# Performance work log

Hardware: AMD Instinct MI355X
Metric: run time of the kernel (lower is better)

## Reference

```python
import jax, jax.numpy as jnp
import numpy as np

N_NODES = 100000
N_EDGES = 800000
N_GRAPHS = 4000
EMB = 128      # node_emb_dims
HID = 256      # hidden_dims
FP = 2048      # fingerprint_dims
FIELD_DIMS = {"atom_type": 120, "degree": 12, "charge": 10}


def setup_inputs() -> dict:
    key = jax.random.key(0)
    ks = iter(jax.random.split(key, 40))
    p = lambda shape: jax.random.normal(next(ks), shape, dtype=jnp.float32) * 0.02
    inp = {
        "atom_idx": jax.random.randint(next(ks), (N_NODES,), 0, FIELD_DIMS["atom_type"]),
        "degree_idx": jax.random.randint(next(ks), (N_NODES,), 0, FIELD_DIMS["degree"]),
        "charge_idx": jax.random.randint(next(ks), (N_NODES,), 0, FIELD_DIMS["charge"]),
        "edge_index": jax.random.randint(next(ks), (2, N_EDGES), 0, N_NODES),
        "batch": jnp.sort(jax.random.randint(next(ks), (N_NODES,), 0, N_GRAPHS)),
        "fingerprint": jax.random.normal(next(ks), (N_GRAPHS, FP), dtype=jnp.float32),
        # FFM projector params
        "emb_atom": p((FIELD_DIMS["atom_type"], EMB)),
        "emb_degree": p((FIELD_DIMS["degree"], EMB)),
        "emb_charge": p((FIELD_DIMS["charge"], EMB)),
        "proj_w1": p((3 * EMB, EMB)), "proj_b1": jnp.zeros((EMB,), jnp.float32),
        "proj_w2": p((EMB, EMB)), "proj_b2": jnp.zeros((EMB,), jnp.float32),
        # fingerprint linear
        "fp_w": p((FP, HID)), "fp_b": jnp.zeros((HID,), jnp.float32),
        # GCN layers
        "conv_w0": p((EMB, HID)), "conv_b0": jnp.zeros((HID,), jnp.float32),
        "conv_w1": p((HID, HID)), "conv_b1": jnp.zeros((HID,), jnp.float32),
        "conv_w2": p((HID, HID)), "conv_b2": jnp.zeros((HID,), jnp.float32),
        "conv_w3": p((HID, HID)), "conv_b3": jnp.zeros((HID,), jnp.float32),
        # head
        "lin1_w": p((2 * HID, HID // 2)), "lin1_b": jnp.zeros((HID // 2,), jnp.float32),
        "lin2_w": p((HID // 2, 1)), "lin2_b": jnp.zeros((1,), jnp.float32),
    }
    return inp


def gcn_conv(x, w, b, src, dst, n):
    # PyG GCNConv: linear, add self-loops, symmetric norm, scatter-add at dst, + bias
    xw = x @ w
    loop = jnp.arange(n)
    src_f = jnp.concatenate([src, loop])
    dst_f = jnp.concatenate([dst, loop])
    deg = jax.ops.segment_sum(jnp.ones_like(dst_f, dtype=x.dtype), dst_f, num_segments=n)
    dinv = jax.lax.rsqrt(deg)  # deg >= 1 thanks to self-loops
    norm = dinv[src_f] * dinv[dst_f]                       # [E+N]
    msg = xw[src_f] * norm[:, None]                        # [E+N, HID]
    return jax.ops.segment_sum(msg, dst_f, num_segments=n) + b


def reference(atom_idx, degree_idx, charge_idx, edge_index, batch, fingerprint,
              emb_atom, emb_degree, emb_charge,
              proj_w1, proj_b1, proj_w2, proj_b2, fp_w, fp_b,
              conv_w0, conv_b0, conv_w1, conv_b1, conv_w2, conv_b2, conv_w3, conv_b3,
              lin1_w, lin1_b, lin2_w, lin2_b):
    # FieldAwareFactorizationMachine projector (vectorized over all nodes)
    e = jnp.concatenate([emb_atom[atom_idx], emb_degree[degree_idx], emb_charge[charge_idx]], axis=-1)
    h = jax.nn.relu(e @ proj_w1 + proj_b1) @ proj_w2 + proj_b2   # [N, EMB]
    src, dst = edge_index[0], edge_index[1]
    for w, b in ((conv_w0, conv_b0), (conv_w1, conv_b1), (conv_w2, conv_b2), (conv_w3, conv_b3)):
        h = jax.nn.relu(gcn_conv(h, w, b, src, dst, N_NODES))
    pooled = jax.ops.segment_sum(h, batch, num_segments=N_GRAPHS)  # scatter sum pooling
    fp_emb = fingerprint @ fp_w + fp_b
    z = jnp.concatenate([fp_emb, pooled], axis=-1)                 # [B, 2*HID]
    z = jax.nn.relu(z @ lin1_w + lin1_b)
    return z @ lin2_w + lin2_b                                     # [B, 1]
```

## Files before the change

kernel.cpp:

```cpp
#include <hip/hip_runtime.h>
#include <stdint.h>

#define NN 100000
#define NE 800000
#define NG 4000
#define NBLK ((NN + 255) / 256)

typedef __attribute__((ext_vector_type(8))) short s16x8;
typedef __attribute__((ext_vector_type(4))) float f32x4;
typedef __attribute__((ext_vector_type(2))) float f32x2;

__device__ __forceinline__ float b2f(unsigned short u) {
    return __uint_as_float(((unsigned int)u) << 16);
}
__device__ __forceinline__ unsigned short f2b(float f) {
    unsigned int x = __float_as_uint(f);
    x = x + 0x7FFFu + ((x >> 16) & 1u);
    return (unsigned short)(x >> 16);
}
__device__ __forceinline__ s16x8 cvt8(const float* __restrict__ p) {
    float4 a = *(const float4*)p;
    float4 b = *(const float4*)(p + 4);
    s16x8 r = {(short)f2b(a.x), (short)f2b(a.y), (short)f2b(a.z), (short)f2b(a.w),
               (short)f2b(b.x), (short)f2b(b.y), (short)f2b(b.z), (short)f2b(b.w)};
    return r;
}

__device__ __forceinline__ void gload16(const void* g, void* l) {
    __builtin_amdgcn_global_load_lds((const __attribute__((address_space(1))) unsigned int*)g,
                                     (__attribute__((address_space(3))) unsigned int*)l, 16, 0, 0);
}

__device__ __forceinline__ void acc8(f32x2* acc, s16x8 r) {
    const unsigned int* u = (const unsigned int*)&r;
#pragma unroll
    for (int q = 0; q < 4; ++q) {
        unsigned int w = u[q];
        f32x2 x;
        x[0] = __uint_as_float(w << 16);
        x[1] = __uint_as_float(w & 0xFFFF0000u);
        asm("v_pk_add_f32 %0, %1, %0" : "+v"(acc[q]) : "v"(x));
    }
}

__global__ void k_count(const int* __restrict__ dst, int* __restrict__ cnt) {
    int e = blockIdx.x * 256 + threadIdx.x;
    if (e < NE) atomicAdd(&cnt[dst[e]], 1);
}

__global__ __launch_bounds__(256) void k_bsum(const int* __restrict__ cnt, int* __restrict__ bsum) {
    __shared__ int s[256];
    int i = blockIdx.x * 256 + threadIdx.x;
    s[threadIdx.x] = (i < NN) ? cnt[i] : 0;
    __syncthreads();
    for (int off = 128; off; off >>= 1) {
        if (threadIdx.x < off) s[threadIdx.x] += s[threadIdx.x + off];
        __syncthreads();
    }
    if (threadIdx.x == 0) bsum[blockIdx.x] = s[0];
}

__global__ __launch_bounds__(512) void k_bscan(const int* __restrict__ bsum, int* __restrict__ bpre) {
    __shared__ int s[512];
    int t = threadIdx.x;
    int v = (t < NBLK) ? bsum[t] : 0;
    s[t] = v;
    __syncthreads();
    for (int off = 1; off < 512; off <<= 1) {
        int u = (t >= off) ? s[t - off] : 0;
        __syncthreads();
        s[t] += u;
        __syncthreads();
    }
    if (t < NBLK) bpre[t] = s[t] - v;
}

__global__ __launch_bounds__(256) void k_rowptr(const int* __restrict__ cnt, const int* __restrict__ bpre,
                                                int* __restrict__ row_ptr, int* __restrict__ cursor,
                                                float* __restrict__ dinv) {
    __shared__ int s[256];
    int t = threadIdx.x;
    int i = blockIdx.x * 256 + t;
    int v = (i < NN) ? cnt[i] : 0;
    s[t] = v;
    __syncthreads();
    for (int off = 1; off < 256; off <<= 1) {
        int u = (t >= off) ? s[t - off] : 0;
        __syncthreads();
        s[t] += u;
        __syncthreads();
    }
    if (i < NN) {
        int excl = bpre[blockIdx.x] + s[t] - v;
        row_ptr[i] = excl;
        cursor[i] = excl;
        dinv[i] = rsqrtf((float)(v + 1));
        if (i == NN - 1) row_ptr[NN] = NE;
    }
}

__global__ void k_fill(const int* __restrict__ src, const int* __restrict__ dst,
                       int* __restrict__ cursor, int* __restrict__ colA) {
    int e = blockIdx.x * 256 + threadIdx.x;
    if (e < NE) {
        int d = dst[e];
        int p = atomicAdd(&cursor[d], 1);
        colA[p] = src[e];
    }
}

struct TArgs {
    const float* src[7];
    unsigned short* dst[7];
    int kn[7];
    int ln[7];
    int off[8];
};

__global__ __launch_bounds__(256) void k_prep(TArgs a) {
    int i = blockIdx.x * 256 + threadIdx.x;
    if (i >= a.off[7]) return;
    int s = 0;
    while (i >= a.off[s + 1]) ++s;
    int j = i - a.off[s];
    int k = j >> a.ln[s], n = j & ((1 << a.ln[s]) - 1);
    a.dst[s][(size_t)n * (a.kn[s] >> a.ln[s]) + k] = f2b(a.src[s][j]);
}

__global__ void k_cvt(const float* __restrict__ src, unsigned short* __restrict__ dst, int n8) {
    int i = blockIdx.x * 256 + threadIdx.x;
    if (i < n8) *(s16x8*)&dst[(size_t)i * 8] = cvt8(&src[(size_t)i * 8]);
}

__global__ __launch_bounds__(256) void k_tab(const float* __restrict__ ea, const float* __restrict__ ed,
                                             const float* __restrict__ ec, const float* __restrict__ w1,
                                             const float* __restrict__ fpb, const float* __restrict__ l1w,
                                             const float* __restrict__ l1b,
                                             float* __restrict__ Tcat, float* __restrict__ b1p) {
    int i = blockIdx.x * 256 + threadIdx.x;
    if (i < 142 * 128) {
        int r = i >> 7, j = i & 127;
        const float* src; int off, lr;
        if (r < 120)      { src = ea; off = 0;   lr = r; }
        else if (r < 132) { src = ed; off = 128; lr = r - 120; }
        else              { src = ec; off = 256; lr = r - 132; }
        float s = 0.f;
        for (int k = 0; k < 128; ++k)
            s = fmaf(src[lr * 128 + k], w1[(off + k) * 128 + j], s);
        Tcat[i] = s;
    } else if (i < 142 * 128 + 128) {
        int j = i - 142 * 128;
        float s = l1b[j];
        for (int c = 0; c < 256; ++c)
            s = fmaf(fpb[c], l1w[c * 128 + j], s);
        b1p[j] = s;
    }
}

__global__ __launch_bounds__(256) void k_emb(const int* __restrict__ ai, const int* __restrict__ di,
                                             const int* __restrict__ ci, const float* __restrict__ Tcat,
                                             const float* __restrict__ b1, unsigned short* __restrict__ h1) {
    int i = blockIdx.x * 256 + threadIdx.x;
    if (i >= NN * 16) return;
    int n = i >> 4, c8 = (i & 15) * 8;
    int a = ai[n], d = di[n], c = ci[n];
    const float* ta = Tcat + a * 128 + c8;
    const float* td = Tcat + (120 + d) * 128 + c8;
    const float* tc = Tcat + (132 + c) * 128 + c8;
    unsigned short o[8];
#pragma unroll
    for (int j = 0; j < 8; ++j) {
        float v = ta[j] + td[j] + tc[j] + b1[c8 + j];
        o[j] = f2b(fmaxf(v, 0.f));
    }
    *(s16x8*)&h1[(size_t)n * 128 + c8] = *(const s16x8*)o;
}

template <bool BIAS, bool RELU, bool CBF16, bool SPLITK, bool PRES>
__global__ __launch_bounds__(256) void k_mmA(
    const unsigned short* __restrict__ A, const unsigned short* __restrict__ Bt,
    void* __restrict__ Cv, const float* __restrict__ bias, const float* __restrict__ pres,
    int M, int N, int K, int kc) {
    __shared__ unsigned short As[2][128 * 32];
    __shared__ unsigned short Bs[2][128 * 32];
    const int tid = threadIdx.x;
    const int row0 = blockIdx.x * 128, col0 = blockIdx.y * 128;
    const int lane = tid & 63, wid = tid >> 6;
    const int wrow = (wid >> 1) * 64, wcol = (wid & 1) * 64;
    const int lr = lane & 15, lk8 = (lane >> 4) * 8;

    const int k0 = SPLITK ? blockIdx.z * kc : 0;
    const int nt = (SPLITK ? kc : K) / 32;

    const int sra = wid * 32 + (lane >> 2);
    const int sca = (lane & 3) * 8;
    const unsigned short* a0 = A + (size_t)min(row0 + sra, M - 1) * K + sca + k0;
    const unsigned short* a1 = A + (size_t)min(row0 + sra + 16, M - 1) * K + sca + k0;
    const unsigned short* b0 = Bt + (size_t)(col0 + sra) * K + sca + k0;
    const unsigned short* b1 = Bt + (size_t)(col0 + sra + 16) * K + sca + k0;
    const int lo0 = (wid * 2 + 0) * 512;
    const int lo1 = (wid * 2 + 1) * 512;

    f32x4 acc[4][4] = {};

    gload16(a0, &As[0][lo0]);
    gload16(a1, &As[0][lo1]);
    gload16(b0, &Bs[0][lo0]);
    gload16(b1, &Bs[0][lo1]);
    __syncthreads();

    int cur = 0;
    for (int t = 0; t < nt; ++t) {
        if (t + 1 < nt) {
            int kb = (t + 1) * 32;
            gload16(a0 + kb, &As[cur ^ 1][lo0]);
            gload16(a1 + kb, &As[cur ^ 1][lo1]);
            gload16(b0 + kb, &Bs[cur ^ 1][lo0]);
            gload16(b1 + kb, &Bs[cur ^ 1][lo1]);
        }
        s16x8 af[4], bfr[4];
#pragma unroll
        for (int f = 0; f < 4; ++f)
            af[f] = *(const s16x8*)&As[cur][(wrow + f * 16 + lr) * 32 + lk8];
#pragma unroll
        for (int f = 0; f < 4; ++f)
            bfr[f] = *(const s16x8*)&Bs[cur][(wcol + f * 16 + lr) * 32 + lk8];
#pragma unroll
        for (int fm = 0; fm < 4; ++fm)
#pragma unroll
            for (int fn = 0; fn < 4; ++fn)
                acc[fm][fn] = __builtin_amdgcn_mfma_f32_16x16x32_bf16(af[fm], bfr[fn], acc[fm][fn], 0, 0, 0);
        __syncthreads();
        cur ^= 1;
    }
#pragma unroll
    for (int fm = 0; fm < 4; ++fm) {
#pragma unroll
        for (int r = 0; r < 4; ++r) {
            int row = row0 + wrow + fm * 16 + (lane >> 4) * 4 + r;
            if (row < M) {
                float pr = PRES ? pres[row] : 1.f;
#pragma unroll
                for (int fn = 0; fn < 4; ++fn) {
                    int col = col0 + wcol + fn * 16 + lr;
                    float v = acc[fm][fn][r];
                    if (SPLITK) {
                        atomicAdd(&((float*)Cv)[(size_t)row * N + col], v);
                    } else {
                        if (BIAS) v += bias[col];
                        if (RELU) v = fmaxf(v, 0.f);
                        if (PRES) v *= pr;
                        if (CBF16) ((unsigned short*)Cv)[(size_t)row * N + col] = f2b(v);
                        else       ((float*)Cv)[(size_t)row * N + col] = v;
                    }
                }
            }
        }
    }
}

template <bool BIAS, bool RELU, bool CBF16, bool PRES>
__global__ __launch_bounds__(512) void k_mmB(
    const unsigned short* __restrict__ A, const unsigned short* __restrict__ Bt,
    void* __restrict__ Cv, const float* __restrict__ bias, const float* __restrict__ pres,
    int M, int K) {
    constexpr int N = 256;
    __shared__ unsigned short As[2][128 * 32];
    __shared__ unsigned short Bs[2][256 * 32];
    const int tid = threadIdx.x;
    const int row0 = blockIdx.x * 128;
    const int lane = tid & 63, wid = tid >> 6;
    const int wrow = (wid >> 2) * 64, wcol = (wid & 3) * 64;
    const int lr = lane & 15, lk8 = (lane >> 4) * 8;

    const int nt = K / 32;

    const int rsub = lane >> 2;
    const int csub = (lane & 3) * 8;
    const unsigned short* ga  = A  + (size_t)min(row0 + wid * 16 + rsub, M - 1) * K + csub;
    const unsigned short* gb0 = Bt + (size_t)(wid * 16 + rsub) * K + csub;
    const unsigned short* gb1 = Bt + (size_t)(128 + wid * 16 + rsub) * K + csub;
    const int la  = wid * 512;
    const int lb0 = wid * 512;
    const int lb1 = (8 + wid) * 512;

    f32x4 acc[4][4] = {};

    gload16(ga, &As[0][la]);
    gload16(gb0, &Bs[0][lb0]);
    gload16(gb1, &Bs[0][lb1]);
    __syncthreads();

    int cur = 0;
    for (int t = 0; t < nt; ++t) {
        if (t + 1 < nt) {
            int kb = (t + 1) * 32;
            gload16(ga + kb, &As[cur ^ 1][la]);
            gload16(gb0 + kb, &Bs[cur ^ 1][lb0]);
            gload16(gb1 + kb, &Bs[cur ^ 1][lb1]);
        }
        s16x8 af[4], bfr[4];
#pragma unroll
        for (int f = 0; f < 4; ++f)
            af[f] = *(const s16x8*)&As[cur][(wrow + f * 16 + lr) * 32 + lk8];
#pragma unroll
        for (int f = 0; f < 4; ++f)
            bfr[f] = *(const s16x8*)&Bs[cur][(wcol + f * 16 + lr) * 32 + lk8];
#pragma unroll
        for (int fm = 0; fm < 4; ++fm)
#pragma unroll
            for (int fn = 0; fn < 4; ++fn)
                acc[fm][fn] = __builtin_amdgcn_mfma_f32_16x16x32_bf16(af[fm], bfr[fn], acc[fm][fn], 0, 0, 0);
        __syncthreads();
        cur ^= 1;
    }
#pragma unroll
    for (int fm = 0; fm < 4; ++fm) {
#pragma unroll
        for (int r = 0; r < 4; ++r) {
            int row = row0 + wrow + fm * 16 + (lane >> 4) * 4 + r;
            if (row < M) {
                float pr = PRES ? pres[row] : 1.f;
#pragma unroll
                for (int fn = 0; fn < 4; ++fn) {
                    int col = wcol + fn * 16 + lr;
                    float v = acc[fm][fn][r];
                    if (BIAS) v += bias[col];
                    if (RELU) v = fmaxf(v, 0.f);
                    if (PRES) v *= pr;
                    if (CBF16) ((unsigned short*)Cv)[(size_t)row * N + col] = f2b(v);
                    else       ((float*)Cv)[(size_t)row * N + col] = v;
                }
            }
        }
    }
}

template <int WPN, bool FUSE>
__global__ __launch_bounds__(256) void k_scat3(const unsigned short* __restrict__ xw,
                                               unsigned short* __restrict__ hout,
                                               const float* __restrict__ dinv,
                                               const int* __restrict__ row_ptr,
                                               const int* __restrict__ colA,
                                               const float* __restrict__ bias) {
    constexpr int W = WPN * 128;
    constexpr int NPW = 4 / WPN;
    const int wid = threadIdx.x >> 6, lane = threadIdx.x & 63;
    const int grp = lane >> 4, li = lane & 15;
    const int v = (blockIdx.x * 4 + wid) * NPW + grp / WPN;
    const int cs = (WPN == 2) ? (grp & 1) * 128 : 0;
    const int c0 = cs + li * 8;

    const float dv = dinv[v];
    s16x8 rs = *(const s16x8*)&xw[(size_t)v * W + c0];

    f32x2 acc[4] = {};
    const int beg = row_ptr[v], end = row_ptr[v + 1];
    int p = beg;
    for (; p + 3 < end; p += 4) {
        int s0 = colA[p], s1 = colA[p + 1], s2 = colA[p + 2], s3 = colA[p + 3];
        s16x8 r0 = *(const s16x8*)&xw[(size_t)s0 * W + c0];
        s16x8 r1 = *(const s16x8*)&xw[(size_t)s1 * W + c0];
        s16x8 r2 = *(const s16x8*)&xw[(size_t)s2 * W + c0];
        s16x8 r3 = *(const s16x8*)&xw[(size_t)s3 * W + c0];
        acc8(acc, r0);
        acc8(acc, r1);
        acc8(acc, r2);
        acc8(acc, r3);
    }
    for (; p < end; ++p) {
        s16x8 r0 = *(const s16x8*)&xw[(size_t)colA[p] * W + c0];
        acc8(acc, r0);
    }

    unsigned short o[8];
#pragma unroll
    for (int j = 0; j < 8; ++j) {
        float a = acc[j >> 1][j & 1];
        a += b2f((unsigned short)rs[j]);
        a *= dv;
        if (FUSE) a = fmaxf(a + bias[c0 + j], 0.f);
        o[j] = f2b(a);
    }
    *(s16x8*)&hout[(size_t)v * W + c0] = *(const s16x8*)o;
}

__global__ void k_bounds(const int* __restrict__ batch, int* __restrict__ gstart) {
    int n = blockIdx.x * 256 + threadIdx.x;
    if (n >= NN) return;
    int b = batch[n];
    if (n == 0) {
        for (int g = 0; g <= b; ++g) gstart[g] = 0;
    } else {
        int pb = batch[n - 1];
        if (pb != b)
            for (int g = pb + 1; g <= b; ++g) gstart[g] = n;
    }
    if (n == NN - 1) {
        for (int g = b + 1; g <= NG; ++g) gstart[g] = NN;
    }
}

__global__ __launch_bounds__(64) void k_pool(const unsigned short* __restrict__ h,
                                             const int* __restrict__ gstart,
                                             unsigned short* __restrict__ pooled) {
    int g = blockIdx.x;
    int lane = threadIdx.x;
    int c0 = lane * 4;
    int beg = gstart[g], end = gstart[g + 1];
    float a0 = 0.f, a1 = 0.f, a2 = 0.f, a3 = 0.f;
    for (int n = beg; n < end; ++n) {
        ushort4 r = *(const ushort4*)&h[(size_t)n * 256 + c0];
        a0 += b2f(r.x); a1 += b2f(r.y); a2 += b2f(r.z); a3 += b2f(r.w);
    }
    ushort4 o;
    o.x = f2b(a0); o.y = f2b(a1); o.z = f2b(a2); o.w = f2b(a3);
    *(ushort4*)&pooled[(size_t)g * 256 + c0] = o;
}

__global__ __launch_bounds__(256) void k_dot(const float* __restrict__ z1,
                                             const float* __restrict__ w2,
                                             const float* __restrict__ b2,
                                             float* __restrict__ out) {
    int wid = threadIdx.x >> 6, lane = threadIdx.x & 63;
    int g = blockIdx.x * 4 + wid;
    float s = fmaxf(z1[(size_t)g * 128 + lane], 0.f) * w2[lane]
            + fmaxf(z1[(size_t)g * 128 + 64 + lane], 0.f) * w2[64 + lane];
#pragma unroll
    for (int off = 32; off; off >>= 1) s += __shfl_xor(s, off);
    if (lane == 0) out[g] = s + b2[0];
}

extern "C" void kernel_launch(void* const* d_in, const int* in_sizes, int n_in,
                              void* d_out, int out_size, void* d_ws, size_t ws_size,
                              hipStream_t stream) {
    const int* atom_idx   = (const int*)d_in[0];
    const int* degree_idx = (const int*)d_in[1];
    const int* charge_idx = (const int*)d_in[2];
    const int* edge_index = (const int*)d_in[3];
    const int* batch      = (const int*)d_in[4];
    const float* fingerprint = (const float*)d_in[5];
    const float* emb_atom   = (const float*)d_in[6];
    const float* emb_degree = (const float*)d_in[7];
    const float* emb_charge = (const float*)d_in[8];
    const float* proj_w1 = (const float*)d_in[9];
    const float* proj_b1 = (const float*)d_in[10];
    const float* proj_w2 = (const float*)d_in[11];
    const float* proj_b2 = (const float*)d_in[12];
    const float* fp_w = (const float*)d_in[13];
    const float* fp_b = (const float*)d_in[14];
    const float* conv_w[4] = {(const float*)d_in[15], (const float*)d_in[17],
                              (const float*)d_in[19], (const float*)d_in[21]};
    const float* conv_b[4] = {(const float*)d_in[16], (const float*)d_in[18],
                              (const float*)d_in[20], (const float*)d_in[22]};
    const float* lin1_w = (const float*)d_in[23];
    const float* lin1_b = (const float*)d_in[24];
    const float* lin2_w = (const float*)d_in[25];
    const float* lin2_b = (const float*)d_in[26];
    float* out = (float*)d_out;

    const int* src = edge_index;
    const int* dst = edge_index + NE;

    char* p = (char*)d_ws;
    auto carve = [&](size_t bytes) { void* r = (void*)p; p += (bytes + 255) & ~(size_t)255; return r; };
    unsigned short* bufA = (unsigned short*)carve((size_t)NN * 256 * 2);
    unsigned short* bufB = (unsigned short*)carve((size_t)NN * 256 * 2);
    int*   cnt     = (int*)carve((size_t)NN * 4);
    float* dinv    = (float*)carve((size_t)NN * 4);
    int*   row_ptr = (int*)carve((size_t)(NN + 1) * 4);
    int*   cursor  = (int*)carve((size_t)(NN + 1) * 4);
    int*   colA    = (int*)carve((size_t)NE * 4);
    int*   gstart  = (int*)carve((size_t)(NG + 1) * 4);
    int*   bsum    = (int*)carve((size_t)NBLK * 4);
    int*   bpre    = (int*)carve((size_t)NBLK * 4);
    unsigned short* w2t  = (unsigned short*)carve((size_t)128 * 128 * 2);
    unsigned short* cwt[4];
    cwt[0] = (unsigned short*)carve((size_t)256 * 128 * 2);
    for (int l = 1; l < 4; ++l) cwt[l] = (unsigned short*)carve((size_t)256 * 256 * 2);
    unsigned short* l1top = (unsigned short*)carve((size_t)128 * 256 * 2);
    unsigned short* l1bot = (unsigned short*)carve((size_t)128 * 256 * 2);
    unsigned short* fpwbf = (unsigned short*)carve((size_t)2048 * 256 * 2);
    unsigned short* wfpt  = (unsigned short*)carve((size_t)128 * 2048 * 2);
    unsigned short* fpbf  = (unsigned short*)carve((size_t)NG * 2048 * 2);
    unsigned short* pooled = (unsigned short*)carve((size_t)NG * 256 * 2);
    float* Tcat   = (float*)carve((size_t)142 * 128 * 4);
    float* b1p    = (float*)carve((size_t)128 * 4);
    float* z1     = (float*)carve((size_t)NG * 128 * 4);

    hipMemsetAsync(cnt, 0, (size_t)NN * 4, stream);
    k_count<<<(NE + 255) / 256, 256, 0, stream>>>(dst, cnt);
    k_bsum<<<NBLK, 256, 0, stream>>>(cnt, bsum);
    k_bscan<<<1, 512, 0, stream>>>(bsum, bpre);
    k_rowptr<<<NBLK, 256, 0, stream>>>(cnt, bpre, row_ptr, cursor, dinv);
    k_fill<<<(NE + 255) / 256, 256, 0, stream>>>(src, dst, cursor, colA);

    {
        TArgs a;
        const float* s7[7] = {proj_w2, conv_w[0], conv_w[1], conv_w[2], conv_w[3],
                              lin1_w, lin1_w + 256 * 128};
        unsigned short* d7[7] = {w2t, cwt[0], cwt[1], cwt[2], cwt[3], l1top, l1bot};
        int kn7[7] = {16384, 32768, 65536, 65536, 65536, 32768, 32768};
        int ln7[7] = {7, 8, 8, 8, 8, 7, 7};
        int o = 0;
        for (int s = 0; s < 7; ++s) { a.src[s] = s7[s]; a.dst[s] = d7[s]; a.kn[s] = kn7[s]; a.ln[s] = ln7[s]; a.off[s] = o; o += kn7[s]; }
        a.off[7] = o;
        k_prep<<<(o + 255) / 256, 256, 0, stream>>>(a);
    }
    k_cvt<<<(2048 * 256 / 8 + 255) / 256, 256, 0, stream>>>(fp_w, fpwbf, 2048 * 256 / 8);
    k_cvt<<<(NG * 2048 / 8 + 255) / 256, 256, 0, stream>>>(fingerprint, fpbf, NG * 2048 / 8);

    k_tab<<<(142 * 128 + 128 + 255) / 256, 256, 0, stream>>>(
        emb_atom, emb_degree, emb_charge, proj_w1, fp_b, lin1_w, lin1_b, Tcat, b1p);

    k_mmA<false, false, true, false, false><<<dim3(1, 16), 256, 0, stream>>>(
        l1top, fpwbf, wfpt, nullptr, nullptr, 128, 2048, 256, 0);

    k_emb<<<(NN * 16 + 255) / 256, 256, 0, stream>>>(
        atom_idx, degree_idx, charge_idx, Tcat, proj_b1, bufA);
    k_mmA<true, false, true, false, true><<<dim3((NN + 127) / 128, 1), 256, 0, stream>>>(
        bufA, w2t, bufB, proj_b2, dinv, NN, 128, 128, 0);

    const int mg = (NN + 127) / 128;

    k_scat3<1, false><<<NN / 16, 256, 0, stream>>>(bufB, bufA, dinv, row_ptr, colA, nullptr);
    k_mmB<true, true, true, false><<<mg, 512, 0, stream>>>(
        bufA, cwt[0], bufB, conv_b[0], nullptr, NN, 128);

    for (int l = 1; l < 4; ++l) {
        k_mmB<false, false, true, true><<<mg, 512, 0, stream>>>(
            bufB, cwt[l], bufA, nullptr, dinv, NN, 256);
        k_scat3<2, true><<<NN / 8, 256, 0, stream>>>(bufA, bufB, dinv, row_ptr, colA, conv_b[l]);
    }

    k_bounds<<<(NN + 255) / 256, 256, 0, stream>>>(batch, gstart);
    k_pool<<<NG, 64, 0, stream>>>(bufB, gstart, pooled);

    k_mmA<true, false, false, false, false><<<dim3((NG + 127) / 128, 1), 256, 0, stream>>>(
        pooled, l1bot, z1, b1p, nullptr, NG, 128, 256, 0);
    k_mmA<false, false, false, true, false><<<dim3((NG + 127) / 128, 1, 4), 256, 0, stream>>>(
        fpbf, wfpt, z1, nullptr, nullptr, NG, 128, 2048, 512);
    k_dot<<<NG / 4, 256, 0, stream>>>(z1, lin2_w, lin2_b, out);
}
```

Baseline: 681.4 us.

## Fuse embedding lookup into projector GEMM and merge small prep kernels

The embedding-sum plus ReLU is now computed directly while staging the A tile of a new MFMA GEMM kernel, so the intermediate h1 buffer is no longer written to and re-read from global memory. proj_b1 is folded into the charge rows of the lookup table. The two fp32-to-bf16 conversion launches are merged into one, and the graph-bounds kernel is replaced by a per-block binary search inside the pooling kernel. The fused GEMM is single-buffered, gathers table rows per K-step and writes scalar bf16 outputs, which may reduce efficiency compared with the earlier tiled GEMM.

```diff
diff --git a/kernel.cpp b/kernel.cpp
--- a/kernel.cpp
+++ b/kernel.cpp
@@ -127,13 +127,20 @@
     a.dst[s][(size_t)n * (a.kn[s] >> a.ln[s]) + k] = f2b(a.src[s][j]);
 }
 
-__global__ void k_cvt(const float* __restrict__ src, unsigned short* __restrict__ dst, int n8) {
+__global__ void k_cvt2(const float* __restrict__ s0, unsigned short* __restrict__ d0, int n80,
+                       const float* __restrict__ s1, unsigned short* __restrict__ d1, int n81) {
     int i = blockIdx.x * 256 + threadIdx.x;
-    if (i < n8) *(s16x8*)&dst[(size_t)i * 8] = cvt8(&src[(size_t)i * 8]);
+    if (i < n80) {
+        *(s16x8*)&d0[(size_t)i * 8] = cvt8(&s0[(size_t)i * 8]);
+    } else if (i < n80 + n81) {
+        int j = i - n80;
+        *(s16x8*)&d1[(size_t)j * 8] = cvt8(&s1[(size_t)j * 8]);
+    }
 }
 
 __global__ __launch_bounds__(256) void k_tab(const float* __restrict__ ea, const float* __restrict__ ed,
                                              const float* __restrict__ ec, const float* __restrict__ w1,
+                                             const float* __restrict__ pb1,
                                              const float* __restrict__ fpb, const float* __restrict__ l1w,
                                              const float* __restrict__ l1b,
                                              float* __restrict__ Tcat, float* __restrict__ b1p) {
@@ -144,7 +151,7 @@
         if (r < 120)      { src = ea; off = 0;   lr = r; }
         else if (r < 132) { src = ed; off = 128; lr = r - 120; }
         else              { src = ec; off = 256; lr = r - 132; }
-        float s = 0.f;
+        float s = (r >= 132) ? pb1[j] : 0.f;
         for (int k = 0; k < 128; ++k)
             s = fmaf(src[lr * 128 + k], w1[(off + k) * 128 + j], s);
         Tcat[i] = s;
@@ -157,23 +164,79 @@
     }
 }
 
-__global__ __launch_bounds__(256) void k_emb(const int* __restrict__ ai, const int* __restrict__ di,
-                                             const int* __restrict__ ci, const float* __restrict__ Tcat,
-                                             const float* __restrict__ b1, unsigned short* __restrict__ h1) {
-    int i = blockIdx.x * 256 + threadIdx.x;
-    if (i >= NN * 16) return;
-    int n = i >> 4, c8 = (i & 15) * 8;
-    int a = ai[n], d = di[n], c = ci[n];
-    const float* ta = Tcat + a * 128 + c8;
-    const float* td = Tcat + (120 + d) * 128 + c8;
-    const float* tc = Tcat + (132 + c) * 128 + c8;
-    unsigned short o[8];
-#pragma unroll
-    for (int j = 0; j < 8; ++j) {
-        float v = ta[j] + td[j] + tc[j] + b1[c8 + j];
-        o[j] = f2b(fmaxf(v, 0.f));
-    }
-    *(s16x8*)&h1[(size_t)n * 128 + c8] = *(const s16x8*)o;
+__global__ __launch_bounds__(256) void k_mmE(
+    const int* __restrict__ ai, const int* __restrict__ di, const int* __restrict__ ci,
+    const float* __restrict__ Tcat, const unsigned short* __restrict__ Bt,
+    unsigned short* __restrict__ C, const float* __restrict__ bias,
+    const float* __restrict__ dinv) {
+    __shared__ unsigned short As[128 * 40];
+    __shared__ unsigned short Bs[128 * 40];
+    const int tid = threadIdx.x;
+    const int row0 = blockIdx.x * 128;
+    const int lane = tid & 63, wid = tid >> 6;
+    const int wrow = (wid >> 1) * 64, wcol = (wid & 1) * 64;
+    const int lr = lane & 15, lk8 = (lane >> 4) * 8;
+    const int sr = tid >> 1, skc = (tid & 1) * 16;
+    const int row = row0 + sr;
+    const int rr = min(row, NN - 1);
+    const float* ta = Tcat + ai[rr] * 128;
+    const float* td = Tcat + (120 + di[rr]) * 128;
+    const float* tc = Tcat + (132 + ci[rr]) * 128;
+
+    f32x4 acc[4][4] = {};
+
+    for (int kb = 0; kb < 128; kb += 32) {
+        if (kb) __syncthreads();
+#pragma unroll
+        for (int c = 0; c < 2; ++c) {
+            int kg = skc + c * 8;
+            int k = kb + kg;
+            float4 a0 = *(const float4*)&ta[k], a1 = *(const float4*)&ta[k + 4];
+            float4 d0 = *(const float4*)&td[k], d1 = *(const float4*)&td[k + 4];
+            float4 e0 = *(const float4*)&tc[k], e1 = *(const float4*)&tc[k + 4];
+            unsigned short o[8];
+            o[0] = f2b(fmaxf(a0.x + d0.x + e0.x, 0.f));
+            o[1] = f2b(fmaxf(a0.y + d0.y + e0.y, 0.f));
+            o[2] = f2b(fmaxf(a0.z + d0.z + e0.z, 0.f));
+            o[3] = f2b(fmaxf(a0.w + d0.w + e0.w, 0.f));
+            o[4] = f2b(fmaxf(a1.x + d1.x + e1.x, 0.f));
+            o[5] = f2b(fmaxf(a1.y + d1.y + e1.y, 0.f));
+            o[6] = f2b(fmaxf(a1.z + d1.z + e1.z, 0.f));
+            o[7] = f2b(fmaxf(a1.w + d1.w + e1.w, 0.f));
+            *(s16x8*)&As[sr * 40 + kg] = *(const s16x8*)o;
+            s16x8 w = *(const s16x8*)&Bt[(size_t)sr * 128 + k];
+            *(s16x8*)&Bs[sr * 40 + kg] = w;
+        }
+        __syncthreads();
+        s16x8 af[4], bfr[4];
+#pragma unroll
+        for (int f = 0; f < 4; ++f)
+            af[f] = *(const s16x8*)&As[(wrow + f * 16 + lr) * 40 + lk8];
+#pragma unroll
+        for (int f = 0; f < 4; ++f)
+            bfr[f] = *(const s16x8*)&Bs[(wcol + f * 16 + lr) * 40 + lk8];
+#pragma unroll
+        for (int fm = 0; fm < 4; ++fm)
+#pragma unroll
+            for (int fn = 0; fn < 4; ++fn)
+                acc[fm][fn] = __builtin_amdgcn_mfma_f32_16x16x32_bf16(af[fm], bfr[fn], acc[fm][fn], 0, 0, 0);
+    }
+#pragma unroll
+    for (int fm = 0; fm < 4; ++fm) {
+#pragma unroll
+        for (int r = 0; r < 4; ++r) {
+            int orow = row0 + wrow + fm * 16 + (lane >> 4) * 4 + r;
+            if (orow < NN) {
+                float pr = dinv[orow];
+#pragma unroll
+                for (int fn = 0; fn < 4; ++fn) {
+                    int col = wcol + fn * 16 + lr;
+                    float v = (acc[fm][fn][r] + bias[col]) * pr;
+                    C[(size_t)orow * 128 + col] = f2b(v);
+                }
+            }
+        }
+    }
 }
 
 template <bool BIAS, bool RELU, bool CBF16, bool SPLITK, bool PRES>
@@ -385,29 +448,24 @@
     *(s16x8*)&hout[(size_t)v * W + c0] = *(const s16x8*)o;
 }
 
-__global__ void k_bounds(const int* __restrict__ batch, int* __restrict__ gstart) {
-    int n = blockIdx.x * 256 + threadIdx.x;
-    if (n >= NN) return;
-    int b = batch[n];
-    if (n == 0) {
-        for (int g = 0; g <= b; ++g) gstart[g] = 0;
-    } else {
-        int pb = batch[n - 1];
-        if (pb != b)
-            for (int g = pb + 1; g <= b; ++g) gstart[g] = n;
-    }
-    if (n == NN - 1) {
-        for (int g = b + 1; g <= NG; ++g) gstart[g] = NN;
-    }
-}
-
-__global__ __launch_bounds__(64) void k_pool(const unsigned short* __restrict__ h,
-                                             const int* __restrict__ gstart,
-                                             unsigned short* __restrict__ pooled) {
+__global__ __launch_bounds__(64) void k_pool2(const unsigned short* __restrict__ h,
+                                              const int* __restrict__ batch,
+                                              unsigned short* __restrict__ pooled) {
+    __shared__ int sb[2];
     int g = blockIdx.x;
+    if (threadIdx.x < 2) {
+        int target = g + threadIdx.x;
+        int lo = 0, hi = NN;
+        while (lo < hi) {
+            int mid = (lo + hi) >> 1;
+            if (batch[mid] < target) lo = mid + 1; else hi = mid;
+        }
+        sb[threadIdx.x] = lo;
+    }
+    __syncthreads();
+    int beg = sb[0], end = sb[1];
     int lane = threadIdx.x;
     int c0 = lane * 4;
-    int beg = gstart[g], end = gstart[g + 1];
     float a0 = 0.f, a1 = 0.f, a2 = 0.f, a3 = 0.f;
     for (int n = beg; n < end; ++n) {
         ushort4 r = *(const ushort4*)&h[(size_t)n * 256 + c0];
@@ -471,7 +529,6 @@
     int*   row_ptr = (int*)carve((size_t)(NN + 1) * 4);
     int*   cursor  = (int*)carve((size_t)(NN + 1) * 4);
     int*   colA    = (int*)carve((size_t)NE * 4);
-    int*   gstart  = (int*)carve((size_t)(NG + 1) * 4);
     int*   bsum    = (int*)carve((size_t)NBLK * 4);
     int*   bpre    = (int*)carve((size_t)NBLK * 4);
     unsigned short* w2t  = (unsigned short*)carve((size_t)128 * 128 * 2);
@@ -507,21 +564,20 @@
         a.off[7] = o;
         k_prep<<<(o + 255) / 256, 256, 0, stream>>>(a);
     }
-    k_cvt<<<(2048 * 256 / 8 + 255) / 256, 256, 0, stream>>>(fp_w, fpwbf, 2048 * 256 / 8);
-    k_cvt<<<(NG * 2048 / 8 + 255) / 256, 256, 0, stream>>>(fingerprint, fpbf, NG * 2048 / 8);
+    {
+        int n80 = 2048 * 256 / 8, n81 = NG * 2048 / 8;
+        k_cvt2<<<(n80 + n81 + 255) / 256, 256, 0, stream>>>(fp_w, fpwbf, n80, fingerprint, fpbf, n81);
+    }
 
     k_tab<<<(142 * 128 + 128 + 255) / 256, 256, 0, stream>>>(
-        emb_atom, emb_degree, emb_charge, proj_w1, fp_b, lin1_w, lin1_b, Tcat, b1p);
+        emb_atom, emb_degree, emb_charge, proj_w1, proj_b1, fp_b, lin1_w, lin1_b, Tcat, b1p);
 
     k_mmA<false, false, true, false, false><<<dim3(1, 16), 256, 0, stream>>>(
         l1top, fpwbf, wfpt, nullptr, nullptr, 128, 2048, 256, 0);
 
-    k_emb<<<(NN * 16 + 255) / 256, 256, 0, stream>>>(
-        atom_idx, degree_idx, charge_idx, Tcat, proj_b1, bufA);
-    k_mmA<true, false, true, false, true><<<dim3((NN + 127) / 128, 1), 256, 0, stream>>>(
-        bufA, w2t, bufB, proj_b2, dinv, NN, 128, 128, 0);
-
     const int mg = (NN + 127) / 128;
+
+    k_mmE<<<mg, 256, 0, stream>>>(atom_idx, degree_idx, charge_idx, Tcat, w2t, bufB, proj_b2, dinv);
 
     k_scat3<1, false><<<NN / 16, 256, 0, stream>>>(bufB, bufA, dinv, row_ptr, colA, nullptr);
     k_mmB<true, true, true, false><<<mg, 512, 0, stream>>>(
@@ -533,8 +589,7 @@
         k_scat3<2, true><<<NN / 8, 256, 0, stream>>>(bufA, bufB, dinv, row_ptr, colA, conv_b[l]);
     }
 
-    k_bounds<<<(NN + 255) / 256, 256, 0, stream>>>(batch, gstart);
-    k_pool<<<NG, 64, 0, stream>>>(bufB, gstart, pooled);
+    k_pool2<<<NG, 64, 0, stream>>>(bufB, batch, pooled);
 
     k_mmA<true, false, false, false, false><<<dim3((NG + 127) / 128, 1), 256, 0, stream>>>(
         pooled, l1bot, z1, b1p, nullptr, NG, 128, 256, 0);
```

New measurement: 677.4 us. No clear change (-0.6%).
